# Optimization experiments

Hardware: AMD Instinct MI355X
Metric: run time of the kernel (lower is better)

The kernel has to match this reference:

```python
import jax, jax.numpy as jnp
import numpy as np

G_CRYSTALS = 64   # number of crystals in the batch
N_ATOMS = 64      # atoms per crystal (dense n^2 edge block per crystal)
N_HEADS = 8
HEAD_DIM = 64


def _make_edges(g, n):
    # dense all-pairs (i, j) within each crystal; atoms of crystal c occupy [c*n, (c+1)*n)
    base = np.arange(g, dtype=np.int32)[:, None, None] * n   # (G,1,1)
    idx = np.arange(n, dtype=np.int32)
    e0 = np.broadcast_to(base + idx[None, :, None], (g, n, n)).reshape(-1)  # query index
    e1 = np.broadcast_to(base + idx[None, None, :], (g, n, n)).reshape(-1)  # key index
    return jnp.asarray(np.stack([e0, e1], axis=0))  # (2, M)


def setup_inputs() -> dict:
    key = jax.random.key(0)
    k0, k1, k2, k3, k4 = jax.random.split(key, 5)
    N = G_CRYSTALS * N_ATOMS                 # 4096 atoms total
    M = G_CRYSTALS * N_ATOMS * N_ATOMS       # 262144 edges
    q = jax.random.normal(k0, (N, N_HEADS, HEAD_DIM), jnp.float32)
    k = jax.random.normal(k1, (N, N_HEADS, HEAD_DIM), jnp.float32)
    v = jax.random.normal(k2, (N, N_HEADS, HEAD_DIM), jnp.float32)
    attn_weights = jax.random.normal(k3, (M, N_HEADS), jnp.float32)          # per-edge additive bias
    values = jax.random.normal(k4, (M, N_HEADS, HEAD_DIM), jnp.float32) * 0.1  # per-edge fused value term
    edges = _make_edges(G_CRYSTALS, N_ATOMS)
    return {"q": q, "k": k, "v": v, "attn_weights": attn_weights,
            "values": values, "edges": edges}


def reference(q, k, v, attn_weights, values, edges):
    # Faithful to the norm_func_mode==0 ('default') fallback path of
    # _scaled_dot_product_attention: per-edge logits, softmax over keys per
    # query (within each crystal's dense block), fused value term.
    N, H, Dh = q.shape
    e0, e1 = edges[0], edges[1]
    scale = 1.0 / jnp.sqrt(jnp.asarray(Dh, q.dtype))
    # per-edge attention logits: (M, H)
    a = jnp.einsum('mhd,mhd->mh', q[e0] * scale, k[e1]) + attn_weights
    # stable softmax over edges sharing the same query index e0
    m = jax.ops.segment_max(a, e0, num_segments=N)      # (N, H)
    p = jnp.exp(a - m[e0])                              # (M, H)
    denom = jax.ops.segment_sum(p, e0, num_segments=N)  # (N, H)
    w = p / denom[e0]                                   # (M, H)
    # output[i] = sum_j w[ij] * (v[j] + values[ij])
    out = jax.ops.segment_sum(w[:, :, None] * (v[e1] + values), e0, num_segments=N)
    return out  # (N, H, Dh)
```

## Files before the change

### kernel.cpp

```cpp
#include <hip/hip_runtime.h>


#define NH 8
#define HD 64
#define ROWSTRIDE 68

typedef float f4 __attribute__((ext_vector_type(4)));

__global__ __launch_bounds__(1024, 8)
void attn_weights_kernel(const float* __restrict__ q,
                         const float* __restrict__ k,
                         const float* __restrict__ v,
                         const float* __restrict__ aw,
                         float* __restrict__ wbuf,
                         float* __restrict__ out) {
    const int c = blockIdx.x & 63;
    const int h = blockIdx.x >> 6;
    const int t = threadIdx.x;

    __shared__ __align__(16) float sq[64][ROWSTRIDE];
    __shared__ __align__(16) float sk[64][ROWSTRIDE];
    __shared__ __align__(16) float sv[64][ROWSTRIDE];
    __shared__ __align__(16) float sa[64][ROWSTRIDE];

    {
        const size_t rowbase = ((size_t)c * 64) * (NH * HD) + (size_t)h * HD;
        const int row = t >> 4;
        const int col = (t & 15) * 4;
        const size_t goff = (size_t)row * (NH * HD) + col;
        *(float4*)&sq[row][col] = *(const float4*)(q + rowbase + goff);
        *(float4*)&sk[row][col] = *(const float4*)(k + rowbase + goff);
        *(float4*)&sv[row][col] = *(const float4*)(v + rowbase + goff);

        const float* ag = aw + ((size_t)c * 4096) * NH + h;
        #pragma unroll
        for (int s = 0; s < 4; ++s) {
            int idx = t + 1024 * s;
            sa[idx >> 6][idx & 63] = ag[(size_t)idx * NH];
        }
    }
    __syncthreads();

    {
        const int w = t >> 6;
        const int i = t & 63;
        const int jbase = w * 4;
        float acc[4];
        #pragma unroll
        for (int jj = 0; jj < 4; ++jj) acc[jj] = 0.f;
        #pragma unroll 4
        for (int d4 = 0; d4 < 16; ++d4) {
            float4 qv = *(const float4*)&sq[i][d4 * 4];
            #pragma unroll
            for (int jj = 0; jj < 4; ++jj) {
                float4 kv = *(const float4*)&sk[jbase + jj][d4 * 4];
                acc[jj] += qv.x * kv.x + qv.y * kv.y + qv.z * kv.z + qv.w * kv.w;
            }
        }
        #pragma unroll
        for (int jj = 0; jj < 4; ++jj)
            sa[i][jbase + jj] = acc[jj] * 0.125f + sa[i][jbase + jj];
    }
    __syncthreads();

    {
        const int r  = t >> 4;
        const int jb = (t & 15) * 4;
        float a0 = sa[r][jb + 0], a1 = sa[r][jb + 1];
        float a2 = sa[r][jb + 2], a3 = sa[r][jb + 3];
        float mx = fmaxf(fmaxf(a0, a1), fmaxf(a2, a3));
        mx = fmaxf(mx, __shfl_xor(mx, 1));
        mx = fmaxf(mx, __shfl_xor(mx, 2));
        mx = fmaxf(mx, __shfl_xor(mx, 4));
        mx = fmaxf(mx, __shfl_xor(mx, 8));
        float p0 = __expf(a0 - mx), p1 = __expf(a1 - mx);
        float p2 = __expf(a2 - mx), p3 = __expf(a3 - mx);
        float sum = p0 + p1 + p2 + p3;
        sum += __shfl_xor(sum, 1);
        sum += __shfl_xor(sum, 2);
        sum += __shfl_xor(sum, 4);
        sum += __shfl_xor(sum, 8);
        const float inv = 1.0f / sum;
        sa[r][jb + 0] = p0 * inv;
        sa[r][jb + 1] = p1 * inv;
        sa[r][jb + 2] = p2 * inv;
        sa[r][jb + 3] = p3 * inv;
    }
    __syncthreads();

    {
        float4 wv = *(const float4*)&sa[t >> 4][(t & 15) * 4];
        *(float4*)(wbuf + (((size_t)c * NH + h) * 4096) + (size_t)t * 4) = wv;
    }

    {
        const int w    = t >> 6;
        const int lane = t & 63;
        const int e    = lane >> 4;
        const int dq   = lane & 15;
        const int i    = 4 * w + e;
        float4 acc = make_float4(0.f, 0.f, 0.f, 0.f);
        #pragma unroll 8
        for (int j = 0; j < 64; ++j) {
            float  p  = sa[i][j];
            float4 sj = *(const float4*)&sv[j][dq * 4];
            acc.x += p * sj.x;
            acc.y += p * sj.y;
            acc.z += p * sj.z;
            acc.w += p * sj.w;
        }
        float* ob = out + ((size_t)(c * 64 + i)) * (NH * HD) + (size_t)h * HD + dq * 4;
        *(float4*)ob = acc;
    }
}

__global__ __launch_bounds__(1024, 8)
void attn_values_kernel(const float* __restrict__ values,
                        const float* __restrict__ wbuf,
                        float* __restrict__ out) {
    const int c  = blockIdx.x >> 3;
    const int ic = blockIdx.x & 7;
    const int t  = threadIdx.x;

    __shared__ float sw[8][64][NH + 1];

    {
        const int h  = t >> 7;
        const int r  = t & 127;
        const int il = r >> 4;
        const int j0 = (r & 15) * 4;
        const float* src = wbuf + (((size_t)c * NH + h) * 64 + (ic * 8 + il)) * 64 + j0;
        float4 wv = *(const float4*)src;
        sw[il][j0 + 0][h] = wv.x;
        sw[il][j0 + 1][h] = wv.y;
        sw[il][j0 + 2][h] = wv.z;
        sw[il][j0 + 3][h] = wv.w;
    }
    __syncthreads();

    const int wv_  = t >> 6;
    const int lane = t & 63;
    const int il   = wv_ >> 1;
    const int half = wv_ & 1;
    const int h    = half * 4 + (lane >> 4);
    const int dq   = lane & 15;
    const int i    = ic * 8 + il;

    const float* vrow = values
        + ((size_t)(c * 4096 + i * 64)) * (NH * HD)
        + (size_t)h * HD + dq * 4;

    float4 acc = make_float4(0.f, 0.f, 0.f, 0.f);
    #pragma unroll 8
    for (int j = 0; j < 64; ++j) {
        f4 val = __builtin_nontemporal_load(
                     (const f4*)(vrow + (size_t)j * (NH * HD)));
        float p = sw[il][j][h];
        acc.x += p * val.x;
        acc.y += p * val.y;
        acc.z += p * val.z;
        acc.w += p * val.w;
    }

    float* ob = out + ((size_t)(c * 64 + i)) * (NH * HD) + (size_t)h * HD + dq * 4;
    float4 o = *(const float4*)ob;
    o.x += acc.x; o.y += acc.y; o.z += acc.z; o.w += acc.w;
    *(float4*)ob = o;
}

extern "C" void kernel_launch(void* const* d_in, const int* in_sizes, int n_in,
                              void* d_out, int out_size, void* d_ws, size_t ws_size,
                              hipStream_t stream) {
    const float* q      = (const float*)d_in[0];
    const float* k      = (const float*)d_in[1];
    const float* v      = (const float*)d_in[2];
    const float* aw     = (const float*)d_in[3];
    const float* values = (const float*)d_in[4];
    float* out  = (float*)d_out;
    float* wbuf = (float*)d_ws;

    dim3 block(1024);
    hipLaunchKernelGGL(attn_weights_kernel, dim3(512), block, 0, stream,
                       q, k, v, aw, wbuf, out);
    hipLaunchKernelGGL(attn_values_kernel, dim3(512), block, 0, stream,
                       values, wbuf, out);
}
```

Measured before the change: 690.3 us.

## Stream values contiguously per query row with cross-wavefront LDS reduction

```diff
diff --git a/kernel.cpp b/kernel.cpp
--- a/kernel.cpp
+++ b/kernel.cpp
@@ -122,50 +122,57 @@
     const int ic = blockIdx.x & 7;
     const int t  = threadIdx.x;
 
-    __shared__ float sw[8][64][NH + 1];
+    __shared__ float sw[8][64][NH];
+    __shared__ __align__(16) float4 red[8][128];
 
-    {
-        const int h  = t >> 7;
-        const int r  = t & 127;
-        const int il = r >> 4;
-        const int j0 = (r & 15) * 4;
-        const float* src = wbuf + (((size_t)c * NH + h) * 64 + (ic * 8 + il)) * 64 + j0;
-        float4 wv = *(const float4*)src;
-        sw[il][j0 + 0][h] = wv.x;
-        sw[il][j0 + 1][h] = wv.y;
-        sw[il][j0 + 2][h] = wv.z;
-        sw[il][j0 + 3][h] = wv.w;
+    #pragma unroll
+    for (int s = 0; s < 4; ++s) {
+        int u  = t + 1024 * s;
+        int h  = u >> 9;
+        int il = (u >> 6) & 7;
+        int j  = u & 63;
+        sw[il][j][h] = wbuf[(((size_t)c * NH + h) * 64 + (ic * 8 + il)) * 64 + j];
     }
     __syncthreads();
 
-    const int wv_  = t >> 6;
-    const int lane = t & 63;
-    const int il   = wv_ >> 1;
-    const int half = wv_ & 1;
-    const int h    = half * 4 + (lane >> 4);
-    const int dq   = lane & 15;
-    const int i    = ic * 8 + il;
+    const int e  = t >> 7;
+    const int h  = (t >> 4) & 7;
+    const int dq = t & 15;
 
-    const float* vrow = values
-        + ((size_t)(c * 4096 + i * 64)) * (NH * HD)
-        + (size_t)h * HD + dq * 4;
+    const float* region = values
+        + ((size_t)(c * 4096 + ic * 8 * 64)) * (NH * HD);
 
-    float4 acc = make_float4(0.f, 0.f, 0.f, 0.f);
-    #pragma unroll 8
-    for (int j = 0; j < 64; ++j) {
-        f4 val = __builtin_nontemporal_load(
-                     (const f4*)(vrow + (size_t)j * (NH * HD)));
-        float p = sw[il][j][h];
-        acc.x += p * val.x;
-        acc.y += p * val.y;
-        acc.z += p * val.z;
-        acc.w += p * val.w;
+    for (int il = 0; il < 8; ++il) {
+        const float* rowp = region + (size_t)il * 64 * (NH * HD) + (size_t)t * 4;
+        float4 acc = make_float4(0.f, 0.f, 0.f, 0.f);
+        #pragma unroll
+        for (int chunk = 0; chunk < 8; ++chunk) {
+            f4 val = *(const f4*)(rowp + (size_t)chunk * 4096);
+            float p = sw[il][chunk * 8 + e][h];
+            acc.x += p * val.x;
+            acc.y += p * val.y;
+            acc.z += p * val.z;
+            acc.w += p * val.w;
+        }
+        red[e][t & 127] = *(float4*)&acc;
+        __syncthreads();
+        if (t < 128) {
+            float4 s0 = red[0][t], s1 = red[1][t], s2 = red[2][t], s3 = red[3][t];
+            float4 s4 = red[4][t], s5 = red[5][t], s6 = red[6][t], s7 = red[7][t];
+            float4 s;
+            s.x = ((s0.x + s1.x) + (s2.x + s3.x)) + ((s4.x + s5.x) + (s6.x + s7.x));
+            s.y = ((s0.y + s1.y) + (s2.y + s3.y)) + ((s4.y + s5.y) + (s6.y + s7.y));
+            s.z = ((s0.z + s1.z) + (s2.z + s3.z)) + ((s4.z + s5.z) + (s6.z + s7.z));
+            s.w = ((s0.w + s1.w) + (s2.w + s3.w)) + ((s4.w + s5.w) + (s6.w + s7.w));
+            const int hh = t >> 4, dd = t & 15;
+            float* ob = out + ((size_t)(c * 64 + ic * 8 + il)) * (NH * HD)
+                            + (size_t)hh * HD + dd * 4;
+            float4 o = *(const float4*)ob;
+            o.x += s.x; o.y += s.y; o.z += s.z; o.w += s.w;
+            *(float4*)ob = o;
+        }
+        __syncthreads();
     }
-
-    float* ob = out + ((size_t)(c * 64 + i)) * (NH * HD) + (size_t)h * HD + dq * 4;
-    float4 o = *(const float4*)ob;
-    o.x += acc.x; o.y += acc.y; o.z += acc.z; o.w += acc.w;
-    *(float4*)ob = o;
 }
 
 extern "C" void kernel_launch(void* const* d_in, const int* in_sizes, int n_in,
```

Result: slower. 713.4 us (+3.3%).
